# Optimization experiments

Hardware: AMD Instinct MI355X
Metric: run time of the kernel (lower is better)

The kernel has to match this reference:

```python
import jax, jax.numpy as jnp
import numpy as np
import math

CHANNELS = 512
N_HEADS = 8
K_CH = CHANNELS // N_HEADS            # 64 per-head dim
ROPE_D = int(K_CH * 0.5)              # 32 dims get RoPE, rest pass through
BASE = 10000


def _rope(x):
    # x: [b, h, t, dk]; rotate first ROPE_D dims (half-split style, matching the torch module)
    d = ROPE_D
    t = x.shape[2]
    theta = 1.0 / (BASE ** (jnp.arange(0, d, 2, dtype=jnp.float32) / d))      # [d/2]
    ang = jnp.arange(t, dtype=jnp.float32)[:, None] * theta[None, :]          # [t, d/2]
    ang = jnp.concatenate([ang, ang], axis=-1)                                # [t, d]
    cos = jnp.cos(ang)[None, None, :, :].astype(x.dtype)
    sin = jnp.sin(ang)[None, None, :, :].astype(x.dtype)
    x_rope, x_pass = x[..., :d], x[..., d:]
    neg_half = jnp.concatenate([-x_rope[..., d // 2:], x_rope[..., :d // 2]], axis=-1)
    return jnp.concatenate([x_rope * cos + neg_half * sin, x_pass], axis=-1)


def _split_heads(y):
    # [b, (h c), t] -> [b, h, t, c]
    b, _, t = y.shape
    return y.reshape(b, N_HEADS, K_CH, t).transpose(0, 1, 3, 2)


def setup_inputs() -> dict:
    key = jax.random.key(0)
    ks = jax.random.split(key, 10)
    B, T = 8, 1024
    w_scale = 1.0 / math.sqrt(CHANNELS)
    return {
        "x": jax.random.normal(ks[0], (B, CHANNELS, T), jnp.float32),
        "c": jax.random.normal(ks[1], (B, CHANNELS, T), jnp.float32),
        "Wq": jax.random.normal(ks[2], (CHANNELS, CHANNELS), jnp.float32) * w_scale,
        "bq": jax.random.normal(ks[3], (CHANNELS,), jnp.float32) * 0.02,
        "Wk": jax.random.normal(ks[4], (CHANNELS, CHANNELS), jnp.float32) * w_scale,
        "bk": jax.random.normal(ks[5], (CHANNELS,), jnp.float32) * 0.02,
        "Wv": jax.random.normal(ks[6], (CHANNELS, CHANNELS), jnp.float32) * w_scale,
        "bv": jax.random.normal(ks[7], (CHANNELS,), jnp.float32) * 0.02,
        "Wo": jax.random.normal(ks[8], (CHANNELS, CHANNELS), jnp.float32) * w_scale,
        "bo": jax.random.normal(ks[9], (CHANNELS,), jnp.float32) * 0.02,
    }


def reference(x, c, Wq, bq, Wk, bk, Wv, bv, Wo, bo):
    # 1x1 Conv1d == per-timestep linear over channels
    q = jnp.einsum('oc,bct->bot', Wq, x) + bq[None, :, None]
    k = jnp.einsum('oc,bct->bot', Wk, c) + bk[None, :, None]
    v = jnp.einsum('oc,bct->bot', Wv, c) + bv[None, :, None]

    q = _rope(_split_heads(q))            # [b,h,t,ck]
    k = _rope(_split_heads(k))            # [b,h,s,ck]
    v = _split_heads(v)                   # [b,h,s,ck]

    scale = 1.0 / math.sqrt(K_CH)
    scores = jnp.einsum('bhtc,bhsc->bhts', q, k) * scale
    p_attn = jax.nn.softmax(scores, axis=-1)       # dropout p=0 -> identity
    out = jnp.einsum('bhts,bhsc->bhtc', p_attn, v)

    b, _, t, _ = out.shape
    out = out.transpose(0, 1, 3, 2).reshape(b, CHANNELS, t)   # [b, (h c), t]
    return jnp.einsum('oc,bct->bot', Wo, out) + bo[None, :, None]
```

## Files before the change

kernel.cpp:

```cpp
#include <hip/hip_runtime.h>

typedef __bf16 bf16x8 __attribute__((ext_vector_type(8)));
typedef float  f32x4  __attribute__((ext_vector_type(4)));

__device__ __forceinline__ unsigned short f2bf(float f){
    union { float f; unsigned u; } v; v.f = f;
    v.u += 0x7fffu + ((v.u >> 16) & 1u);
    return (unsigned short)(v.u >> 16);
}
__device__ __forceinline__ void gl2lds16(const unsigned short* g, unsigned short* l){
    __builtin_amdgcn_global_load_lds(
        (const __attribute__((address_space(1))) void*)g,
        (__attribute__((address_space(3))) void*)l, 16, 0, 0);
}

__global__ __launch_bounds__(256) void transpose_cvt(const float* __restrict__ x, const float* __restrict__ c,
                                                     const float* __restrict__ w0, const float* __restrict__ w1,
                                                     const float* __restrict__ w2, const float* __restrict__ w3,
                                                     unsigned short* __restrict__ xt, unsigned short* __restrict__ ct,
                                                     unsigned short* __restrict__ o0, unsigned short* __restrict__ o1,
                                                     unsigned short* __restrict__ o2, unsigned short* __restrict__ o3){
    __shared__ float tile[64][72];
    const int z = blockIdx.z;
    if (z == 16){
        int fid = (blockIdx.x * 8 + blockIdx.y) * 256 + threadIdx.x;
        const float* in; unsigned short* out;
        switch (fid >> 13){
            case 0: in = w0; out = o0; break;
            case 1: in = w1; out = o1; break;
            case 2: in = w2; out = o2; break;
            default: in = w3; out = o3; break;
        }
        int off = (fid & 8191) * 32;
        #pragma unroll
        for (int j = 0; j < 8; j++){
            float4 v = *(const float4*)(in + off + j*4);
            ushort4 o; o.x = f2bf(v.x); o.y = f2bf(v.y); o.z = f2bf(v.z); o.w = f2bf(v.w);
            *(ushort4*)(out + off + j*4) = o;
        }
        return;
    }
    const float* in = (z < 8) ? x : c;
    unsigned short* out = (z < 8) ? xt : ct;
    const int b = z & 7;
    const int t0 = blockIdx.x * 64, c0 = blockIdx.y * 64;
    const int tid = threadIdx.x;
    {
        int r = tid >> 2, q = (tid & 3) * 16;
        const float* src = in + ((size_t)b * 512 + c0 + r) * 1024 + t0 + q;
        #pragma unroll
        for (int j = 0; j < 4; j++)
            *(float4*)&tile[r][q + j*4] = ((const float4*)src)[j];
    }
    __syncthreads();
    {
        int tr = tid >> 2, cj = (tid & 3) * 16;
        unsigned pw[8];
        #pragma unroll
        for (int j = 0; j < 8; j++){
            unsigned lo = f2bf(tile[cj + 2*j    ][tr]);
            unsigned hi = f2bf(tile[cj + 2*j + 1][tr]);
            pw[j] = lo | (hi << 16);
        }
        unsigned short* dst = out + ((size_t)b * 1024 + t0 + tr) * 512 + c0 + cj;
        uint4 q0 = {pw[0], pw[1], pw[2], pw[3]};
        uint4 q1 = {pw[4], pw[5], pw[6], pw[7]};
        ((uint4*)dst)[0] = q0;
        ((uint4*)dst)[1] = q1;
    }
}

__device__ __forceinline__ void gemm_mainloop(const unsigned short* __restrict__ A,
                                              const unsigned short* __restrict__ Bm,
                                              unsigned short* a_s, unsigned short* b_s,
                                              int m0, int n0, int tid, f32x4 acc[4][4]){
    const int wave = tid >> 6, lane = tid & 63;
    const int l15 = lane & 15, l4 = lane >> 4;
    const int mw = (wave >> 1) * 64, nw = (wave & 1) * 64;
    const int r8 = lane >> 3, c8l = lane & 7;
    const int csw = (c8l ^ r8) * 8;
    const int rp = l15 & 7;

    for (int k0 = 0; k0 < 512; k0 += 64){
        #pragma unroll
        for (int i = 0; i < 4; i++){
            int rg = i * 4 + wave;
            int row = rg * 8 + r8;
            gl2lds16(A  + (size_t)(m0 + row) * 512 + k0 + csw, a_s + rg * 512);
            gl2lds16(Bm + (size_t)(n0 + row) * 512 + k0 + csw, b_s + rg * 512);
        }
        __syncthreads();
        #pragma unroll
        for (int kk = 0; kk < 2; kk++){
            bf16x8 af[4], bfr[4];
            #pragma unroll
            for (int mt = 0; mt < 4; mt++)
                af[mt] = *(const bf16x8*)&a_s[(mw + mt*16 + l15)*64 + (((kk*4) + l4) ^ rp)*8];
            #pragma unroll
            for (int ct = 0; ct < 4; ct++)
                bfr[ct] = *(const bf16x8*)&b_s[(nw + ct*16 + l15)*64 + (((kk*4) + l4) ^ rp)*8];
            #pragma unroll
            for (int mt = 0; mt < 4; mt++)
                #pragma unroll
                for (int ct = 0; ct < 4; ct++)
                    acc[mt][ct] = __builtin_amdgcn_mfma_f32_16x16x32_bf16(
                        af[mt], bfr[ct], acc[mt][ct], 0, 0, 0);
        }
        __syncthreads();
    }
}

__global__ __launch_bounds__(256) void qkv_gemm(const unsigned short* __restrict__ xt,
                                                const unsigned short* __restrict__ ct,
                                                const unsigned short* __restrict__ wq,
                                                const unsigned short* __restrict__ wk,
                                                const unsigned short* __restrict__ wv,
                                                const float* __restrict__ bq_,
                                                const float* __restrict__ bk_,
                                                const float* __restrict__ bv_,
                                                unsigned short* __restrict__ qt,
                                                unsigned short* __restrict__ kt,
                                                unsigned short* __restrict__ vct){
    __shared__ unsigned short a_s[128*64];
    __shared__ unsigned short b_s[128*64];
    const int z = blockIdx.y, bid = blockIdx.x;
    const unsigned short *A, *Bm;
    int m0, n0;
    if (z == 0){ A = xt; Bm = wq; m0 = (bid >> 2)*128; n0 = (bid & 3)*128; }
    else if (z == 1){ A = ct; Bm = wk; m0 = (bid >> 2)*128; n0 = (bid & 3)*128; }
    else { A = wv; Bm = ct; m0 = (bid & 3)*128; n0 = (bid >> 2)*128; }
    const int tid = threadIdx.x;
    const int wave = tid >> 6, lane = tid & 63;
    const int l15 = lane & 15, l4 = lane >> 4;
    const int mw = (wave >> 1) * 64, nw = (wave & 1) * 64;
    const f32x4 vzero = {0.f, 0.f, 0.f, 0.f};
    f32x4 acc[4][4];
    #pragma unroll
    for (int i = 0; i < 4; i++)
        #pragma unroll
        for (int j = 0; j < 4; j++) acc[i][j] = vzero;

    gemm_mainloop(A, Bm, a_s, b_s, m0, n0, tid, acc);

    if (z < 2){
        unsigned short* out = (z == 0) ? qt : kt;
        const float* bias = (z == 0) ? bq_ : bk_;
        const float osc = (z == 0) ? 0.1803368801111137f : 1.0f;
        float bv4[4];
        #pragma unroll
        for (int ct2 = 0; ct2 < 4; ct2++) bv4[ct2] = bias[n0 + nw + ct2*16 + l15];
        const float theta = __powf(10000.0f, -(float)l15 * (1.0f / 16.0f));
        #pragma unroll
        for (int mt = 0; mt < 4; mt++){
            #pragma unroll
            for (int rr = 0; rr < 4; rr++){
                int row = m0 + mw + mt*16 + l4*4 + rr;
                int t = row & 1023;
                float v[4];
                #pragma unroll
                for (int ct2 = 0; ct2 < 4; ct2++) v[ct2] = acc[mt][ct2][rr] + bv4[ct2];
                float sn, cn;
                __sincosf((float)t * theta, &sn, &cn);
                float r0 = v[0] * cn - v[1] * sn;
                float r1 = v[1] * cn + v[0] * sn;
                v[0] = r0; v[1] = r1;
                #pragma unroll
                for (int ct2 = 0; ct2 < 4; ct2++)
                    out[(size_t)row * 512 + n0 + nw + ct2*16 + l15] = f2bf(v[ct2] * osc);
            }
        }
    } else {
        #pragma unroll
        for (int mt = 0; mt < 4; mt++){
            #pragma unroll
            for (int rr = 0; rr < 4; rr++){
                int row = m0 + mw + mt*16 + l4*4 + rr;
                float bb = bv_[row];
                #pragma unroll
                for (int ct2 = 0; ct2 < 4; ct2++){
                    int n = n0 + nw + ct2*16 + l15;
                    size_t oaddr = (size_t)(n >> 10) * 524288 + (size_t)row * 1024 + (n & 1023);
                    vct[oaddr] = f2bf(acc[mt][ct2][rr] + bb);
                }
            }
        }
    }
}

__global__ __launch_bounds__(256) void gemm_o(const unsigned short* __restrict__ wo,
                                              const unsigned short* __restrict__ attnT,
                                              const float* __restrict__ bo,
                                              float* __restrict__ out){
    __shared__ unsigned short a_s[64*64];
    __shared__ unsigned short b_s[128*64];
    const int m0 = blockIdx.x * 64, n0 = blockIdx.y * 128;
    const int tid = threadIdx.x;
    const int wave = tid >> 6, lane = tid & 63;
    const int l15 = lane & 15, l4 = lane >> 4;
    const int nw = wave * 32;
    const int r8 = lane >> 3, c8l = lane & 7;
    const int csw = (c8l ^ r8) * 8;
    const int rp = l15 & 7;
    const f32x4 vzero = {0.f, 0.f, 0.f, 0.f};
    f32x4 acc[4][2];
    #pragma unroll
    for (int i = 0; i < 4; i++){ acc[i][0] = vzero; acc[i][1] = vzero; }

    for (int k0 = 0; k0 < 512; k0 += 64){
        #pragma unroll
        for (int i = 0; i < 2; i++){
            int rg = wave * 2 + i;
            gl2lds16(wo + (size_t)(m0 + rg*8 + r8) * 512 + k0 + csw, a_s + rg * 512);
        }
        #pragma unroll
        for (int i = 0; i < 4; i++){
            int rg = wave * 4 + i;
            gl2lds16(attnT + (size_t)(n0 + rg*8 + r8) * 512 + k0 + csw, b_s + rg * 512);
        }
        __syncthreads();
        #pragma unroll
        for (int kk = 0; kk < 2; kk++){
            bf16x8 af[4], bfr[2];
            #pragma unroll
            for (int mt = 0; mt < 4; mt++)
                af[mt] = *(const bf16x8*)&a_s[(mt*16 + l15)*64 + (((kk*4) + l4) ^ rp)*8];
            #pragma unroll
            for (int ct = 0; ct < 2; ct++)
                bfr[ct] = *(const bf16x8*)&b_s[(nw + ct*16 + l15)*64 + (((kk*4) + l4) ^ rp)*8];
            #pragma unroll
            for (int mt = 0; mt < 4; mt++)
                #pragma unroll
                for (int ct = 0; ct < 2; ct++)
                    acc[mt][ct] = __builtin_amdgcn_mfma_f32_16x16x32_bf16(
                        af[mt], bfr[ct], acc[mt][ct], 0, 0, 0);
        }
        __syncthreads();
    }

    #pragma unroll
    for (int mt = 0; mt < 4; mt++){
        #pragma unroll
        for (int rr = 0; rr < 4; rr++){
            int row = m0 + mt*16 + l4*4 + rr;
            float bb = bo[row];
            #pragma unroll
            for (int ct2 = 0; ct2 < 2; ct2++){
                int n = n0 + nw + ct2*16 + l15;
                size_t oaddr = (size_t)(n >> 10) * 524288 + (size_t)row * 1024 + (n & 1023);
                out[oaddr] = acc[mt][ct2][rr] + bb;
            }
        }
    }
}

__global__ __launch_bounds__(256, 2) void flash_attn(const unsigned short* __restrict__ qt,
                                                     const unsigned short* __restrict__ kt,
                                                     const unsigned short* __restrict__ vct,
                                                     unsigned short* __restrict__ attnT){
    __shared__ unsigned short k_s[2][64*64];
    __shared__ unsigned short v_s[2][64*64];
    __shared__ unsigned short p_s[4][2][16*72];
    const int bhq = blockIdx.x;
    const int bh = bhq & 63, b = bh >> 3, h = bh & 7;
    const int q0 = (bhq >> 6) * 128;
    const int tid = threadIdx.x, wave = tid >> 6, lane = tid & 63;
    const int l15 = lane & 15, l4 = lane >> 4;
    const int r8 = lane >> 3, c8l = lane & 7;
    const int csw = (c8l ^ r8) * 8;
    const int rp = l15 & 7;
    const f32x4 vzero = {0.f, 0.f, 0.f, 0.f};
    const unsigned short* kbase = kt  + (size_t)(b*1024)*512 + h*64;
    const unsigned short* vbase = vct + (size_t)(b*512 + h*64)*1024;

    bf16x8 qf[2][2];
    #pragma unroll
    for (int st = 0; st < 2; st++)
        #pragma unroll
        for (int kh = 0; kh < 2; kh++)
            qf[st][kh] = *(const bf16x8*)(qt + (size_t)(b*1024 + q0 + wave*32 + st*16 + l15)*512
                                             + h*64 + kh*32 + l4*8);
    f32x4 o_acc[2][4], l_acc[2];
    #pragma unroll
    for (int st = 0; st < 2; st++){
        l_acc[st] = vzero;
        #pragma unroll
        for (int dt = 0; dt < 4; dt++) o_acc[st][dt] = vzero;
    }
    const __bf16 one_bf = (__bf16)1.0f;
    const bf16x8 ones = {one_bf, one_bf, one_bf, one_bf, one_bf, one_bf, one_bf, one_bf};

    auto stage = [&](int tile, int buf){
        const int s0n = tile * 64;
        #pragma unroll
        for (int i = 0; i < 2; i++){
            int rg = i * 4 + wave;
            int row = rg * 8 + r8;
            gl2lds16(kbase + (size_t)(s0n + row)*512 + csw, &k_s[buf][rg*512]);
            gl2lds16(vbase + (size_t)row*1024 + s0n + csw, &v_s[buf][rg*512]);
        }
    };
    stage(0, 0);
    __syncthreads();

    for (int it = 0; it < 16; ++it){
        const int cur = it & 1;
        if (it < 15) stage(it + 1, cur ^ 1);
        bf16x8 kf[2][4], vf[2][4];
        #pragma unroll
        for (int kh = 0; kh < 2; kh++)
            #pragma unroll
            for (int ct = 0; ct < 4; ct++)
                kf[kh][ct] = *(const bf16x8*)&k_s[cur][(ct*16 + l15)*64 + ((kh*4 + l4) ^ rp)*8];
        #pragma unroll
        for (int sh = 0; sh < 2; sh++)
            #pragma unroll
            for (int dt = 0; dt < 4; dt++)
                vf[sh][dt] = *(const bf16x8*)&v_s[cur][(dt*16 + l15)*64 + ((sh*4 + l4) ^ rp)*8];
        #pragma unroll
        for (int st = 0; st < 2; st++){
            f32x4 sa[4];
            #pragma unroll
            for (int ct = 0; ct < 4; ct++) sa[ct] = vzero;
            #pragma unroll
            for (int kh = 0; kh < 2; kh++)
                #pragma unroll
                for (int ct = 0; ct < 4; ct++)
                    sa[ct] = __builtin_amdgcn_mfma_f32_16x16x32_bf16(kf[kh][ct], qf[st][kh], sa[ct], 0, 0, 0);
            #pragma unroll
            for (int ct = 0; ct < 4; ct++)
                #pragma unroll
                for (int rr = 0; rr < 4; rr++)
                    sa[ct][rr] = exp2f(sa[ct][rr]);
            #pragma unroll
            for (int ct = 0; ct < 4; ct++){
                union { float f; unsigned u; } a0, a1, a2, a3;
                a0.f = sa[ct][0]; a1.f = sa[ct][1]; a2.f = sa[ct][2]; a3.f = sa[ct][3];
                uint2 w;
                w.x = (a0.u >> 16) | (a1.u & 0xffff0000u);
                w.y = (a2.u >> 16) | (a3.u & 0xffff0000u);
                *(uint2*)&p_s[wave][st][l15*72 + ct*16 + l4*4] = w;
            }
            asm volatile("s_waitcnt lgkmcnt(0)" ::: "memory");
            __builtin_amdgcn_sched_barrier(0);
            bf16x8 ap0 = *(const bf16x8*)&p_s[wave][st][l15*72 + l4*8];
            bf16x8 ap1 = *(const bf16x8*)&p_s[wave][st][l15*72 + 32 + l4*8];
            l_acc[st] = __builtin_amdgcn_mfma_f32_16x16x32_bf16(ap0, ones, l_acc[st], 0, 0, 0);
            l_acc[st] = __builtin_amdgcn_mfma_f32_16x16x32_bf16(ap1, ones, l_acc[st], 0, 0, 0);
            #pragma unroll
            for (int dt = 0; dt < 4; dt++){
                o_acc[st][dt] = __builtin_amdgcn_mfma_f32_16x16x32_bf16(ap0, vf[0][dt], o_acc[st][dt], 0, 0, 0);
                o_acc[st][dt] = __builtin_amdgcn_mfma_f32_16x16x32_bf16(ap1, vf[1][dt], o_acc[st][dt], 0, 0, 0);
            }
        }
        __syncthreads();
    }
    #pragma unroll
    for (int st = 0; st < 2; st++){
        float rl[4];
        #pragma unroll
        for (int rr = 0; rr < 4; rr++) rl[rr] = __builtin_amdgcn_rcpf(l_acc[st][rr]);
        #pragma unroll
        for (int dt = 0; dt < 4; dt++)
            #pragma unroll
            for (int rr = 0; rr < 4; rr++){
                int row = q0 + wave*32 + st*16 + l4*4 + rr;
                attnT[(size_t)(b*1024 + row)*512 + h*64 + dt*16 + l15] = f2bf(o_acc[st][dt][rr] * rl[rr]);
            }
    }
}

extern "C" void kernel_launch(void* const* d_in, const int* in_sizes, int n_in,
                              void* d_out, int out_size, void* d_ws, size_t ws_size,
                              hipStream_t stream){
    const float* x  = (const float*)d_in[0];
    const float* c  = (const float*)d_in[1];
    const float* Wq = (const float*)d_in[2];
    const float* bq = (const float*)d_in[3];
    const float* Wk = (const float*)d_in[4];
    const float* bk = (const float*)d_in[5];
    const float* Wv = (const float*)d_in[6];
    const float* bv = (const float*)d_in[7];
    const float* Wo = (const float*)d_in[8];
    const float* bo = (const float*)d_in[9];

    unsigned short* wq_b = (unsigned short*)d_ws;
    unsigned short* wk_b = wq_b + 262144;
    unsigned short* wv_b = wk_b + 262144;
    unsigned short* wo_b = wv_b + 262144;
    unsigned short* xt   = wo_b + 262144;
    unsigned short* ct   = xt  + 4194304;
    unsigned short* qt   = ct  + 4194304;
    unsigned short* kt   = qt  + 4194304;
    unsigned short* vct  = kt  + 4194304;
    unsigned short* attnT = xt;

    transpose_cvt<<<dim3(16, 8, 17), 256, 0, stream>>>(x, c, Wq, Wk, Wv, Wo,
                                                       xt, ct, wq_b, wk_b, wv_b, wo_b);
    qkv_gemm<<<dim3(256, 3), 256, 0, stream>>>(xt, ct, wq_b, wk_b, wv_b, bq, bk, bv, qt, kt, vct);
    flash_attn<<<dim3(512), 256, 0, stream>>>(qt, kt, vct, attnT);
    gemm_o<<<dim3(8, 64), 256, 0, stream>>>(wo_b, attnT, bo, (float*)d_out);
}
```

Measured before the change: 165.0 us.

## Double-buffer LDS tiles in projection GEMMs and swizzle QKV block order

The QKV and output-projection GEMM main loops now use two LDS buffers, prefetching the next K-slice with global_load_lds while MFMAs run on the current one. This is meant to overlap global-to-LDS copy latency with compute instead of stalling at a barrier each iteration. The QKV grid also remaps block indices so neighbouring blocks share operand tiles for better L2 reuse. LDS use per block doubles, which can lower occupancy. The loop bodies' trailing barrier is not visible, so correctness of the buffer reuse depends on it.

```diff
diff --git a/kernel.cpp b/kernel.cpp
--- a/kernel.cpp
+++ b/kernel.cpp
@@ -81,24 +81,35 @@
     const int csw = (c8l ^ r8) * 8;
     const int rp = l15 & 7;
 
-    for (int k0 = 0; k0 < 512; k0 += 64){
+    auto stage = [&](int k0, int buf){
+        unsigned short* as = a_s + buf * (128*64);
+        unsigned short* bs = b_s + buf * (128*64);
         #pragma unroll
         for (int i = 0; i < 4; i++){
             int rg = i * 4 + wave;
             int row = rg * 8 + r8;
-            gl2lds16(A  + (size_t)(m0 + row) * 512 + k0 + csw, a_s + rg * 512);
-            gl2lds16(Bm + (size_t)(n0 + row) * 512 + k0 + csw, b_s + rg * 512);
-        }
-        __syncthreads();
+            gl2lds16(A  + (size_t)(m0 + row) * 512 + k0 + csw, as + rg * 512);
+            gl2lds16(Bm + (size_t)(n0 + row) * 512 + k0 + csw, bs + rg * 512);
+        }
+    };
+
+    stage(0, 0);
+    __syncthreads();
+
+    for (int t = 0; t < 8; t++){
+        const int buf = t & 1;
+        if (t < 7) stage((t + 1) * 64, buf ^ 1);
+        const unsigned short* as = a_s + buf * (128*64);
+        const unsigned short* bs = b_s + buf * (128*64);
         #pragma unroll
         for (int kk = 0; kk < 2; kk++){
             bf16x8 af[4], bfr[4];
             #pragma unroll
             for (int mt = 0; mt < 4; mt++)
-                af[mt] = *(const bf16x8*)&a_s[(mw + mt*16 + l15)*64 + (((kk*4) + l4) ^ rp)*8];
+                af[mt] = *(const bf16x8*)&as[(mw + mt*16 + l15)*64 + (((kk*4) + l4) ^ rp)*8];
             #pragma unroll
             for (int ct = 0; ct < 4; ct++)
-                bfr[ct] = *(const bf16x8*)&b_s[(nw + ct*16 + l15)*64 + (((kk*4) + l4) ^ rp)*8];
+                bfr[ct] = *(const bf16x8*)&bs[(nw + ct*16 + l15)*64 + (((kk*4) + l4) ^ rp)*8];
             #pragma unroll
             for (int mt = 0; mt < 4; mt++)
                 #pragma unroll
@@ -121,9 +132,11 @@
                                                 unsigned short* __restrict__ qt,
                                                 unsigned short* __restrict__ kt,
                                                 unsigned short* __restrict__ vct){
-    __shared__ unsigned short a_s[128*64];
-    __shared__ unsigned short b_s[128*64];
-    const int z = blockIdx.y, bid = blockIdx.x;
+    __shared__ unsigned short a_s[2*128*64];
+    __shared__ unsigned short b_s[2*128*64];
+    const int z = blockIdx.y;
+    const int xr = blockIdx.x;
+    const int bid = (xr & 7) * 32 + (xr >> 3);
     const unsigned short *A, *Bm;
     int m0, n0;
     if (z == 0){ A = xt; Bm = wq; m0 = (bid >> 2)*128; n0 = (bid & 3)*128; }
@@ -191,8 +204,8 @@
                                               const unsigned short* __restrict__ attnT,
                                               const float* __restrict__ bo,
                                               float* __restrict__ out){
-    __shared__ unsigned short a_s[64*64];
-    __shared__ unsigned short b_s[128*64];
+    __shared__ unsigned short a_s[2*64*64];
+    __shared__ unsigned short b_s[2*128*64];
     const int m0 = blockIdx.x * 64, n0 = blockIdx.y * 128;
     const int tid = threadIdx.x;
     const int wave = tid >> 6, lane = tid & 63;
@@ -206,27 +219,38 @@
     #pragma unroll
     for (int i = 0; i < 4; i++){ acc[i][0] = vzero; acc[i][1] = vzero; }
 
-    for (int k0 = 0; k0 < 512; k0 += 64){
+    auto stage = [&](int k0, int buf){
+        unsigned short* as = a_s + buf * (64*64);
+        unsigned short* bs = b_s + buf * (128*64);
         #pragma unroll
         for (int i = 0; i < 2; i++){
             int rg = wave * 2 + i;
-            gl2lds16(wo + (size_t)(m0 + rg*8 + r8) * 512 + k0 + csw, a_s + rg * 512);
+            gl2lds16(wo + (size_t)(m0 + rg*8 + r8) * 512 + k0 + csw, as + rg * 512);
         }
         #pragma unroll
         for (int i = 0; i < 4; i++){
             int rg = wave * 4 + i;
-            gl2lds16(attnT + (size_t)(n0 + rg*8 + r8) * 512 + k0 + csw, b_s + rg * 512);
-        }
-        __syncthreads();
+            gl2lds16(attnT + (size_t)(n0 + rg*8 + r8) * 512 + k0 + csw, bs + rg * 512);
+        }
+    };
+
+    stage(0, 0);
+    __syncthreads();
+
+    for (int t = 0; t < 8; t++){
+        const int buf = t & 1;
+        if (t < 7) stage((t + 1) * 64, buf ^ 1);
+        const unsigned short* as = a_s + buf * (64*64);
+        const unsigned short* bs = b_s + buf * (128*64);
         #pragma unroll
         for (int kk = 0; kk < 2; kk++){
             bf16x8 af[4], bfr[2];
             #pragma unroll
             for (int mt = 0; mt < 4; mt++)
-                af[mt] = *(const bf16x8*)&a_s[(mt*16 + l15)*64 + (((kk*4) + l4) ^ rp)*8];
+                af[mt] = *(const bf16x8*)&as[(mt*16 + l15)*64 + (((kk*4) + l4) ^ rp)*8];
             #pragma unroll
             for (int ct = 0; ct < 2; ct++)
-                bfr[ct] = *(const bf16x8*)&b_s[(nw + ct*16 + l15)*64 + (((kk*4) + l4) ^ rp)*8];
+                bfr[ct] = *(const bf16x8*)&bs[(nw + ct*16 + l15)*64 + (((kk*4) + l4) ^ rp)*8];
             #pragma unroll
             for (int mt = 0; mt < 4; mt++)
                 #pragma unroll
```

Result: no change. 164.6 us (-0.3%).
